# Kernel optimization log

Hardware: AMD Instinct MI355X
Metric: run time of the kernel (lower is better)

## Reference

```python
import jax, jax.numpy as jnp
import numpy as np

WIDTH = 2048
NUM_HEADS = 16
HEAD_DIM = WIDTH // NUM_HEADS  # 128
ROPE_DIMS = HEAD_DIM // 2      # 64, partial rotary
WINDOW = 512
ROPE_BASE = 10000.0
NEG_INF = -1e9


def apply_rope(x, dims, offset=0, base=ROPE_BASE):
    # x: [B, H, L, hd]; non-traditional (half-split) rotary on first `dims` dims.
    L = x.shape[2]
    half = dims // 2
    pos = (offset + jnp.arange(L)).astype(x.dtype)                     # [L]
    inv_freq = jnp.exp(-jnp.log(jnp.asarray(base, x.dtype)) * (jnp.arange(0, dims, 2).astype(x.dtype) / dims))  # [half]
    theta = pos[:, None] * inv_freq[None, :]                           # [L, half]
    cos = jnp.cos(theta)[None, None]                                   # [1,1,L,half]
    sin = jnp.sin(theta)[None, None]
    x1 = x[..., :half]
    x2 = x[..., half:dims]
    rest = x[..., dims:]
    rx1 = x1 * cos - x2 * sin
    rx2 = x1 * sin + x2 * cos
    return jnp.concatenate([rx1, rx2, rest], axis=-1)


def setup_inputs() -> dict:
    key = jax.random.key(0)
    ks = jax.random.split(key, 6)
    B, L, D, hd = 2, 2048, WIDTH, HEAD_DIM
    x = jax.random.normal(ks[0], (B, L, D), dtype=jnp.float32)
    Wq = jax.random.normal(ks[1], (D, D), dtype=jnp.float32) * 0.02
    Wk = jax.random.normal(ks[2], (D, hd), dtype=jnp.float32) * 0.02
    Wv = jax.random.normal(ks[3], (D, hd), dtype=jnp.float32) * 0.02
    Wo = jax.random.normal(ks[4], (D, D), dtype=jnp.float32) * 0.02
    bo = jax.random.normal(ks[5], (D,), dtype=jnp.float32) * 0.02
    return {"x": x, "Wq": Wq, "Wk": Wk, "Wv": Wv, "Wo": Wo, "bo": bo}


def reference(x, Wq, Wk, Wv, Wo, bo):
    B, L, D = x.shape
    H, hd = NUM_HEADS, HEAD_DIM
    scale = hd ** (-0.5)

    q = (x @ Wq).reshape(B, L, H, hd).transpose(0, 2, 1, 3)   # [B,H,L,hd]
    k = (x @ Wk).reshape(B, L, 1, hd).transpose(0, 2, 1, 3)   # [B,1,L,hd] (MQA)
    v = (x @ Wv).reshape(B, L, 1, hd).transpose(0, 2, 1, 3)

    q = apply_rope(q, ROPE_DIMS)
    k = apply_rope(k, ROPE_DIMS)

    # sliding-window causal mask: attend iff 0 <= i - j < WINDOW
    i = jnp.arange(L)[:, None]
    j = jnp.arange(L)[None, :]
    allowed = (i - j >= 0) & (i - j < WINDOW)                  # [L,L]
    mask = jnp.where(allowed, 0.0, NEG_INF).astype(x.dtype)

    scores = jnp.einsum("bhqd,bkd->bhqk", q, k[:, 0]) * scale  # [B,H,L,L]
    scores = scores + mask[None, None]
    attn = jax.nn.softmax(scores, axis=-1)
    out = jnp.einsum("bhqk,bkd->bhqd", attn, v[:, 0])          # [B,H,L,hd]
    out = out.transpose(0, 2, 1, 3).reshape(B, L, D)
    return out @ Wo + bo
```

## Files before the change

### kernel.cpp

```cpp
#include <hip/hip_runtime.h>
#include <hip/hip_bf16.h>
#include <stdint.h>


typedef float  f32x4  __attribute__((ext_vector_type(4)));
typedef __bf16 bf16x8 __attribute__((ext_vector_type(8)));

#define ASYNC_LD16(gp, lp)                                                     \
  __builtin_amdgcn_global_load_lds(                                            \
      (__attribute__((address_space(1))) void*)(gp),                           \
      (__attribute__((address_space(3))) void*)(lp), 16, 0, 0)

__global__ __launch_bounds__(256) void prep_all(
    const float* __restrict__ x, __hip_bfloat16* __restrict__ xb,
    const float* __restrict__ Wq, const float* __restrict__ Wk,
    const float* __restrict__ Wv, const float* __restrict__ Wo,
    __hip_bfloat16* __restrict__ wqkvT, __hip_bfloat16* __restrict__ woT) {
  __shared__ float t[32][33];
  int bid = blockIdx.x;
  if (bid < 8192) {
    const int i = bid * 256 + threadIdx.x;
    const float4 v = ((const float4*)x)[i];
    __align__(8) __hip_bfloat16 o[4] = {
        __float2bfloat16(v.x), __float2bfloat16(v.y),
        __float2bfloat16(v.z), __float2bfloat16(v.w)};
    *(uint2*)(xb + (size_t)i * 4) = *(uint2*)o;
    return;
  }
  bid -= 8192;
  const float* src;
  __hip_bfloat16* dst;
  int C, cb, rb;
  if (bid < 4096) {
    src = Wq; dst = wqkvT; C = 2048; cb = bid & 63; rb = bid >> 6;
  } else if (bid < 4352) {
    const int l = bid - 4096;
    src = Wk; dst = wqkvT + 2048ull * 2048; C = 128; cb = l & 3; rb = l >> 2;
  } else if (bid < 4608) {
    const int l = bid - 4352;
    src = Wv; dst = wqkvT + 2176ull * 2048; C = 128; cb = l & 3; rb = l >> 2;
  } else {
    const int l = bid - 4608;
    src = Wo; dst = woT; C = 2048; cb = l & 63; rb = l >> 6;
  }
  const int c0 = cb * 32, r0 = rb * 32;
  const int xx = threadIdx.x & 31, y = threadIdx.x >> 5;
#pragma unroll
  for (int i = 0; i < 32; i += 8)
    t[y + i][xx] = src[(size_t)(r0 + y + i) * C + c0 + xx];
  __syncthreads();
#pragma unroll
  for (int i = 0; i < 32; i += 8)
    dst[(size_t)(c0 + y + i) * 2048 + r0 + xx] = __float2bfloat16(t[xx][y + i]);
}

__device__ __forceinline__ void xcd_remap(int& bx, int& by) {
  const int nwg = gridDim.x * gridDim.y;
  const int flat = blockIdx.y * gridDim.x + blockIdx.x;
  const int cpx = nwg >> 3;
  const int nid = (flat & 7) * cpx + (flat >> 3);
  bx = nid % gridDim.x;
  by = nid / gridDim.x;
}

__device__ __forceinline__ void gemm_core64(const __bf16* __restrict__ A,
                                            const __bf16* __restrict__ BT,
                                            int K, int m0, int n0, __bf16* As,
                                            __bf16* Bs, f32x4 (&acc)[2][4]) {
  const int tid = threadIdx.x;
  const int wave = tid >> 6;
  const int lane = tid & 63;
  const int wm = (wave & 1) * 32;
  const int wn = (wave >> 1) * 64;
  const int ln = lane & 15;
  const int quad = lane >> 4;
  const int rdoff = (quad ^ ((ln >> 1) & 3)) * 8;

  size_t goffA[2];
  int ldsoffA[2];
#pragma unroll
  for (int i = 0; i < 2; i++) {
    const int cidx = (wave * 2 + i) * 64 + lane;
    const int p = cidx >> 8;
    const int pidx = cidx & 255;
    const int row = pidx >> 2;
    const int cc = pidx & 3;
    const int cg = cc ^ ((row >> 1) & 3);
    goffA[i] = (size_t)row * K + p * 32 + cg * 8;
    ldsoffA[i] = (wave * 2 + i) * 512;
  }
  size_t goffB[4];
  int ldsoffB[4];
#pragma unroll
  for (int i = 0; i < 4; i++) {
    const int cidx = (wave * 4 + i) * 64 + lane;
    const int p = cidx >> 9;
    const int pidx = cidx & 511;
    const int row = pidx >> 2;
    const int cc = pidx & 3;
    const int cg = cc ^ ((row >> 1) & 3);
    goffB[i] = (size_t)row * K + p * 32 + cg * 8;
    ldsoffB[i] = (wave * 4 + i) * 512;
  }
  const __bf16* Abase = A + (size_t)m0 * K;
  const __bf16* Bbase = BT + (size_t)n0 * K;

  for (int k0 = 0; k0 < K; k0 += 64) {
#pragma unroll
    for (int i = 0; i < 2; i++)
      ASYNC_LD16(Abase + k0 + goffA[i], As + ldsoffA[i]);
#pragma unroll
    for (int i = 0; i < 4; i++)
      ASYNC_LD16(Bbase + k0 + goffB[i], Bs + ldsoffB[i]);
    __syncthreads();
    bf16x8 af[2][2], bf[4][2];
#pragma unroll
    for (int i = 0; i < 2; i++)
#pragma unroll
      for (int p = 0; p < 2; p++)
        af[i][p] = *(const bf16x8*)&As[p * 2048 + (wm + i * 16 + ln) * 32 + rdoff];
#pragma unroll
    for (int j = 0; j < 4; j++)
#pragma unroll
      for (int p = 0; p < 2; p++)
        bf[j][p] = *(const bf16x8*)&Bs[p * 4096 + (wn + j * 16 + ln) * 32 + rdoff];
#pragma unroll
    for (int p = 0; p < 2; p++)
#pragma unroll
      for (int i = 0; i < 2; i++)
#pragma unroll
        for (int j = 0; j < 4; j++)
          acc[i][j] = __builtin_amdgcn_mfma_f32_16x16x32_bf16(af[i][p], bf[j][p],
                                                              acc[i][j], 0, 0, 0);
    __syncthreads();
  }
}

__global__ __launch_bounds__(256) void gemm_qkv(
    const __bf16* __restrict__ A, const __bf16* __restrict__ BT,
    __hip_bfloat16* __restrict__ qd, __hip_bfloat16* __restrict__ kd,
    __hip_bfloat16* __restrict__ vtd, int K) {
  __shared__ __align__(16) __bf16 As[2 * 2048];
  __shared__ __align__(16) __bf16 Bs[2 * 4096];
  int bx, by;
  xcd_remap(bx, by);
  const int m0 = by * 64;
  const int n0 = bx * 128;
  f32x4 acc[2][4];
  const f32x4 zero = {0.f, 0.f, 0.f, 0.f};
#pragma unroll
  for (int i = 0; i < 2; i++)
#pragma unroll
    for (int j = 0; j < 4; j++) acc[i][j] = zero;
  gemm_core64(A, BT, K, m0, n0, As, Bs, acc);

  const int tid = threadIdx.x;
  const int wave = tid >> 6;
  const int lane = tid & 63;
  const int quad = lane >> 4;
  const int ln = lane & 15;
  const int wm = (wave & 1) * 32;
  const int wn = (wave >> 1) * 64;

  if (n0 == 2176) {
    const int bb = m0 >> 11;
    const int mloc = m0 & 2047;
#pragma unroll
    for (int i = 0; i < 2; i++) {
      const int rb = mloc + wm + i * 16 + quad * 4;
#pragma unroll
      for (int j = 0; j < 4; j++) {
        const int col = wn + j * 16 + ln;
        __align__(8) __hip_bfloat16 t4[4];
#pragma unroll
        for (int r = 0; r < 4; r++) t4[r] = __float2bfloat16(acc[i][j][r]);
        *(uint2*)(vtd + ((size_t)(bb * 128 + col)) * 2048 + rb) = *(uint2*)t4;
      }
    }
    return;
  }

  __hip_bfloat16* dst;
  int dstride, dcol;
  if (n0 < 2048) {
    dst = qd; dstride = 2048; dcol = n0;
  } else {
    dst = kd; dstride = 128; dcol = 0;
  }
  const bool dorope = (wn == 0);
  float invf0 = 0.f, invf1 = 0.f;
  if (dorope) {
    invf0 = expf(-0.28782313662425574f * (float)ln);
    invf1 = expf(-0.28782313662425574f * (float)(16 + ln));
  }

#pragma unroll
  for (int i = 0; i < 2; i++) {
#pragma unroll
    for (int r = 0; r < 4; r++) {
      const int row = m0 + wm + i * 16 + quad * 4 + r;
      float o0 = acc[i][0][r], o1 = acc[i][1][r];
      float o2 = acc[i][2][r], o3 = acc[i][3][r];
      if (dorope) {
        const float pos = (float)(row & 2047);
        float s0, c0, s1, c1;
        __sincosf(pos * invf0, &s0, &c0);
        __sincosf(pos * invf1, &s1, &c1);
        const float a0 = o0, b0 = o2, a1 = o1, b1 = o3;
        o0 = a0 * c0 - b0 * s0;
        o2 = a0 * s0 + b0 * c0;
        o1 = a1 * c1 - b1 * s1;
        o3 = a1 * s1 + b1 * c1;
      }
      __hip_bfloat16* rp = dst + (size_t)row * dstride + dcol + wn + ln;
      rp[0]  = __float2bfloat16(o0);
      rp[16] = __float2bfloat16(o1);
      rp[32] = __float2bfloat16(o2);
      rp[48] = __float2bfloat16(o3);
    }
  }
}

__global__ __launch_bounds__(256) void gemm_out(
    const __bf16* __restrict__ A, const __bf16* __restrict__ BT,
    float* __restrict__ C, const float* __restrict__ bias, int N, int K) {
  __shared__ __align__(16) __bf16 As[2 * 2048];
  __shared__ __align__(16) __bf16 Bs[2 * 4096];
  int bx, by;
  xcd_remap(bx, by);
  const int m0 = by * 64;
  const int n0 = bx * 128;
  f32x4 acc[2][4];
  const f32x4 zero = {0.f, 0.f, 0.f, 0.f};
#pragma unroll
  for (int i = 0; i < 2; i++)
#pragma unroll
    for (int j = 0; j < 4; j++) acc[i][j] = zero;
  gemm_core64(A, BT, K, m0, n0, As, Bs, acc);

  const int tid = threadIdx.x;
  const int wave = tid >> 6;
  const int lane = tid & 63;
  const int wm = (wave & 1) * 32;
  const int wn = (wave >> 1) * 64;
  const int lrow = lane & 15;
#pragma unroll
  for (int j = 0; j < 4; j++) {
    const int col = n0 + wn + j * 16 + lrow;
    const float bv = bias[col];
#pragma unroll
    for (int i = 0; i < 2; i++) {
#pragma unroll
      for (int r = 0; r < 4; r++) {
        const int row = m0 + wm + i * 16 + (lane >> 4) * 4 + r;
        C[(size_t)row * N + col] = acc[i][j][r] + bv;
      }
    }
  }
}

__global__ __launch_bounds__(256) void attn_mfma(
    const __bf16* __restrict__ qb,
    const __bf16* __restrict__ kb,
    const __bf16* __restrict__ vtb,
    __hip_bfloat16* __restrict__ o)
{
  __shared__ __align__(16) __bf16 Ks[2][4][64 * 32];
  __shared__ __align__(16) __bf16 Vs[2][2][128 * 32];
  __shared__ __align__(16) __bf16 Ps[4][2][2][512];
  const int tid = threadIdx.x;
  const int wave = tid >> 6;
  const int lane = tid & 63;
  const int quad = lane >> 4;
  const int ln = lane & 15;
  const int bid = blockIdx.x;
  const int q0 = (bid & 15) * 128;
  const int h = (bid >> 4) & 15;
  const int b = bid >> 8;
  const int swr = (ln >> 1) & 3;
  const int rdoff = (quad ^ swr) * 8;

  bf16x8 qf[2][4];
#pragma unroll
  for (int g = 0; g < 2; g++) {
    const __bf16* qrow =
        qb + ((size_t)(b * 2048 + q0 + wave * 32 + g * 16 + ln)) * 2048 + h * 128;
#pragma unroll
    for (int ks = 0; ks < 4; ks++)
      qf[g][ks] = *(const bf16x8*)(qrow + ks * 32 + quad * 8);
  }

  f32x4 oacc[2][8];
  const f32x4 zero = {0.f, 0.f, 0.f, 0.f};
#pragma unroll
  for (int g = 0; g < 2; g++)
#pragma unroll
    for (int nb = 0; nb < 8; nb++) oacc[g][nb] = zero;
  float li[2][4] = {{0.f, 0.f, 0.f, 0.f}, {0.f, 0.f, 0.f, 0.f}};
  const float scale = 0.08838834764831845f;

  const __bf16* kbase = kb + (size_t)b * 2048 * 128;
  const __bf16* vbase = vtb + (size_t)b * 128 * 2048;

  const int key4 = lane >> 2, uu = lane & 3;
  const int sw = (key4 >> 1) & 3;

  auto stage_kv = [&](int t, int bufi) {
    const int jt = q0 - 512 + 64 * t;
#pragma unroll
    for (int i = 0; i < 4; ++i) {
      const int c = wave * 4 + i;
      const int ks = c & 3, keybase = (c >> 2) * 16;
      ASYNC_LD16(kbase + (size_t)(jt + keybase + key4) * 128 + ks * 32 +
                     (uu ^ sw) * 8,
                 &Ks[bufi][ks][keybase * 32]);
    }
#pragma unroll
    for (int i = 0; i < 4; ++i) {
      const int c = wave * 4 + i;
      const int p = c & 1, dbase = (c >> 1) * 16;
      ASYNC_LD16(vbase + (size_t)(dbase + key4) * 2048 + jt + p * 32 +
                     (uu ^ sw) * 8,
                 &Vs[bufi][p][dbase * 32]);
    }
  };

#define SOFTMAX_BODY(MASKED)                                                   \
  _Pragma("unroll") for (int g = 0; g < 2; g++)                                \
  _Pragma("unroll") for (int j = 0; j < 4; j++)                                \
  _Pragma("unroll") for (int r = 0; r < 4; r++) {                              \
    float v = sacc[g][j][r] * scale;                                           \
    if (MASKED) {                                                              \
      const int d0 = (wave * 32 + g * 16 + quad * 4 + r) - (j * 16 + ln);      \
      if (t <= 1 && d0 >= (t << 6)) v = -1e30f;                                \
      if (t >= 8 && d0 < ((t - 8) << 6)) v = -1e30f;                           \
    }                                                                          \
    v = fminf(v, 60.f);                                                        \
    const float p = __expf(v);                                                 \
    li[g][r] += p;                                                             \
    const int ch = (j & 1) * 2 + (ln >> 3);                                    \
    const int swp = (quad * 2 + (r >> 1)) & 3;                                 \
    Ps[wave][g][j >> 1][(quad * 4 + r) * 32 + (ch ^ swp) * 8 + (ln & 7)] =     \
        (__bf16)p;                                                             \
  }

  const int tstart = (q0 >= 512) ? 0 : (512 - q0) / 64;
  int cur = 0;
  stage_kv(tstart, 0);
  for (int t = tstart; t < 10; ++t) {
    __syncthreads();
    if (t + 1 < 10) stage_kv(t + 1, cur ^ 1);

    f32x4 sacc[2][4];
#pragma unroll
    for (int g = 0; g < 2; g++)
#pragma unroll
      for (int j = 0; j < 4; j++) sacc[g][j] = zero;
    __builtin_amdgcn_s_setprio(1);
#pragma unroll
    for (int j = 0; j < 4; j++)
#pragma unroll
      for (int ks = 0; ks < 4; ks++) {
        const bf16x8 kf =
            *(const bf16x8*)&Ks[cur][ks][(j * 16 + ln) * 32 + rdoff];
#pragma unroll
        for (int g = 0; g < 2; g++)
          sacc[g][j] = __builtin_amdgcn_mfma_f32_16x16x32_bf16(
              qf[g][ks], kf, sacc[g][j], 0, 0, 0);
      }
    __builtin_amdgcn_s_setprio(0);

    if (t <= 1 || t >= 8) {
      SOFTMAX_BODY(1)
    } else {
      SOFTMAX_BODY(0)
    }

    const bf16x8 pf00 = *(const bf16x8*)&Ps[wave][0][0][ln * 32 + rdoff];
    const bf16x8 pf01 = *(const bf16x8*)&Ps[wave][0][1][ln * 32 + rdoff];
    const bf16x8 pf10 = *(const bf16x8*)&Ps[wave][1][0][ln * 32 + rdoff];
    const bf16x8 pf11 = *(const bf16x8*)&Ps[wave][1][1][ln * 32 + rdoff];
    __builtin_amdgcn_s_setprio(1);
#pragma unroll
    for (int nb = 0; nb < 8; nb++) {
      const bf16x8 vf0 =
          *(const bf16x8*)&Vs[cur][0][(nb * 16 + ln) * 32 + rdoff];
      const bf16x8 vf1 =
          *(const bf16x8*)&Vs[cur][1][(nb * 16 + ln) * 32 + rdoff];
      oacc[0][nb] = __builtin_amdgcn_mfma_f32_16x16x32_bf16(pf00, vf0,
                                                            oacc[0][nb], 0, 0, 0);
      oacc[0][nb] = __builtin_amdgcn_mfma_f32_16x16x32_bf16(pf01, vf1,
                                                            oacc[0][nb], 0, 0, 0);
      oacc[1][nb] = __builtin_amdgcn_mfma_f32_16x16x32_bf16(pf10, vf0,
                                                            oacc[1][nb], 0, 0, 0);
      oacc[1][nb] = __builtin_amdgcn_mfma_f32_16x16x32_bf16(pf11, vf1,
                                                            oacc[1][nb], 0, 0, 0);
    }
    __builtin_amdgcn_s_setprio(0);
    cur ^= 1;
  }
#undef SOFTMAX_BODY

#pragma unroll
  for (int off = 1; off < 16; off <<= 1)
#pragma unroll
    for (int g = 0; g < 2; g++)
#pragma unroll
      for (int r = 0; r < 4; r++) li[g][r] += __shfl_xor(li[g][r], off);

#pragma unroll
  for (int g = 0; g < 2; g++) {
    __hip_bfloat16* obase =
        o + ((size_t)(b * 2048 + q0 + wave * 32 + g * 16 + quad * 4)) * 2048 +
        h * 128 + ln;
#pragma unroll
    for (int r = 0; r < 4; r++) {
      const float inv = 1.0f / li[g][r];
#pragma unroll
      for (int nb = 0; nb < 8; nb++)
        obase[(size_t)r * 2048 + nb * 16] = __float2bfloat16(oacc[g][nb][r] * inv);
    }
  }
}

extern "C" void kernel_launch(void* const* d_in, const int* in_sizes, int n_in,
                              void* d_out, int out_size, void* d_ws,
                              size_t ws_size, hipStream_t stream) {
  const float* x = (const float*)d_in[0];
  const float* Wq = (const float*)d_in[1];
  const float* Wk = (const float*)d_in[2];
  const float* Wv = (const float*)d_in[3];
  const float* Wo = (const float*)d_in[4];
  const float* bo = (const float*)d_in[5];
  float* out = (float*)d_out;

  char* w = (char*)d_ws;
  auto alloc = [&](size_t bytes) {
    void* p = (void*)w;
    w += (bytes + 255) & ~(size_t)255;
    return p;
  };
  __bf16* xb = (__bf16*)alloc(4096ull * 2048 * 2);
  __hip_bfloat16* wqkvT = (__hip_bfloat16*)alloc(2304ull * 2048 * 2);
  __hip_bfloat16* woT = (__hip_bfloat16*)alloc(2048ull * 2048 * 2);
  __hip_bfloat16* qbuf = (__hip_bfloat16*)alloc(4096ull * 2048 * 2);
  __hip_bfloat16* kbuf = (__hip_bfloat16*)alloc(4096ull * 128 * 2);
  __hip_bfloat16* vtb = (__hip_bfloat16*)alloc(4096ull * 128 * 2);
  __hip_bfloat16* attnb = (__hip_bfloat16*)xb;

  prep_all<<<16896, 256, 0, stream>>>(x, (__hip_bfloat16*)xb, Wq, Wk, Wv, Wo,
                                      wqkvT, woT);

  gemm_qkv<<<dim3(18, 64), 256, 0, stream>>>(xb, (const __bf16*)wqkvT, qbuf,
                                             kbuf, vtb, 2048);

  attn_mfma<<<512, 256, 0, stream>>>((const __bf16*)qbuf, (const __bf16*)kbuf,
                                     (const __bf16*)vtb, attnb);

  gemm_out<<<dim3(16, 64), 256, 0, stream>>>((const __bf16*)attnb,
                                             (const __bf16*)woT, out, bo, 2048,
                                             2048);
}
```

Before: 249.7 us.

## Switch GEMMs to 128x128 tiles with 32x32x16 MFMA and XOR-swizzled LDS

Both projection GEMMs now use 128x128 block tiles instead of 64x128. Each wave computes a 64x64 sub-tile with 32x32x16 bf16 MFMA instructions, and the LDS layout becomes a flat 64-wide row with an XOR swizzle. The epilogues (RoPE, V transpose store, bias add) are remapped to the 32x32 accumulator layout, and the grids are halved in M. The aim is more data reuse per LDS load and fewer MFMA issue slots, at the cost of fewer blocks (576 and 512) and possibly lower occupancy or wave balance on the CUs.

```diff
diff --git a/kernel.cpp b/kernel.cpp
--- a/kernel.cpp
+++ b/kernel.cpp
@@ -3,8 +3,9 @@
 #include <stdint.h>
 
 
-typedef float  f32x4  __attribute__((ext_vector_type(4)));
-typedef __bf16 bf16x8 __attribute__((ext_vector_type(8)));
+typedef float  f32x4   __attribute__((ext_vector_type(4)));
+typedef float  f32x16  __attribute__((ext_vector_type(16)));
+typedef __bf16 bf16x8  __attribute__((ext_vector_type(8)));
 
 #define ASYNC_LD16(gp, lp)                                                     \
   __builtin_amdgcn_global_load_lds(                                            \
@@ -63,75 +64,65 @@
   by = nid / gridDim.x;
 }
 
-__device__ __forceinline__ void gemm_core64(const __bf16* __restrict__ A,
+__device__ __forceinline__ void gemm_core32(const __bf16* __restrict__ A,
                                             const __bf16* __restrict__ BT,
                                             int K, int m0, int n0, __bf16* As,
-                                            __bf16* Bs, f32x4 (&acc)[2][4]) {
+                                            __bf16* Bs, f32x16 (&acc)[2][2]) {
   const int tid = threadIdx.x;
   const int wave = tid >> 6;
   const int lane = tid & 63;
-  const int wm = (wave & 1) * 32;
+  const int wm = (wave & 1) * 64;
   const int wn = (wave >> 1) * 64;
-  const int ln = lane & 15;
-  const int quad = lane >> 4;
-  const int rdoff = (quad ^ ((ln >> 1) & 3)) * 8;
-
-  size_t goffA[2];
-  int ldsoffA[2];
-#pragma unroll
-  for (int i = 0; i < 2; i++) {
-    const int cidx = (wave * 2 + i) * 64 + lane;
-    const int p = cidx >> 8;
-    const int pidx = cidx & 255;
-    const int row = pidx >> 2;
-    const int cc = pidx & 3;
-    const int cg = cc ^ ((row >> 1) & 3);
-    goffA[i] = (size_t)row * K + p * 32 + cg * 8;
-    ldsoffA[i] = (wave * 2 + i) * 512;
-  }
-  size_t goffB[4];
-  int ldsoffB[4];
+  const int l5 = lane & 31;
+  const int half = lane >> 5;
+
+  size_t goff[4];
+  int ldso[4];
 #pragma unroll
   for (int i = 0; i < 4; i++) {
-    const int cidx = (wave * 4 + i) * 64 + lane;
-    const int p = cidx >> 9;
-    const int pidx = cidx & 511;
-    const int row = pidx >> 2;
-    const int cc = pidx & 3;
-    const int cg = cc ^ ((row >> 1) & 3);
-    goffB[i] = (size_t)row * K + p * 32 + cg * 8;
-    ldsoffB[i] = (wave * 4 + i) * 512;
+    const int cidx = i * 256 + tid;
+    const int row = cidx >> 3;
+    const int c = cidx & 7;
+    const int cg = c ^ (row & 7);
+    goff[i] = (size_t)row * K + cg * 8;
+    ldso[i] = cidx * 8;
   }
   const __bf16* Abase = A + (size_t)m0 * K;
   const __bf16* Bbase = BT + (size_t)n0 * K;
 
   for (int k0 = 0; k0 < K; k0 += 64) {
 #pragma unroll
-    for (int i = 0; i < 2; i++)
-      ASYNC_LD16(Abase + k0 + goffA[i], As + ldsoffA[i]);
-#pragma unroll
     for (int i = 0; i < 4; i++)
-      ASYNC_LD16(Bbase + k0 + goffB[i], Bs + ldsoffB[i]);
+      ASYNC_LD16(Abase + k0 + goff[i], As + ldso[i]);
+#pragma unroll
+    for (int i = 0; i < 4; i++)
+      ASYNC_LD16(Bbase + k0 + goff[i], Bs + ldso[i]);
     __syncthreads();
-    bf16x8 af[2][2], bf[4][2];
-#pragma unroll
-    for (int i = 0; i < 2; i++)
-#pragma unroll
-      for (int p = 0; p < 2; p++)
-        af[i][p] = *(const bf16x8*)&As[p * 2048 + (wm + i * 16 + ln) * 32 + rdoff];
-#pragma unroll
-    for (int j = 0; j < 4; j++)
-#pragma unroll
-      for (int p = 0; p < 2; p++)
-        bf[j][p] = *(const bf16x8*)&Bs[p * 4096 + (wn + j * 16 + ln) * 32 + rdoff];
-#pragma unroll
-    for (int p = 0; p < 2; p++)
-#pragma unroll
-      for (int i = 0; i < 2; i++)
-#pragma unroll
-        for (int j = 0; j < 4; j++)
-          acc[i][j] = __builtin_amdgcn_mfma_f32_16x16x32_bf16(af[i][p], bf[j][p],
-                                                              acc[i][j], 0, 0, 0);
+    bf16x8 af[2][4], bf[2][4];
+#pragma unroll
+    for (int fi = 0; fi < 2; fi++) {
+      const int row = wm + fi * 32 + l5;
+      const int sw = row & 7;
+#pragma unroll
+      for (int s = 0; s < 4; s++)
+        af[fi][s] = *(const bf16x8*)&As[row * 64 + ((s * 2 + half) ^ sw) * 8];
+    }
+#pragma unroll
+    for (int fj = 0; fj < 2; fj++) {
+      const int row = wn + fj * 32 + l5;
+      const int sw = row & 7;
+#pragma unroll
+      for (int s = 0; s < 4; s++)
+        bf[fj][s] = *(const bf16x8*)&Bs[row * 64 + ((s * 2 + half) ^ sw) * 8];
+    }
+#pragma unroll
+    for (int s = 0; s < 4; s++)
+#pragma unroll
+      for (int fi = 0; fi < 2; fi++)
+#pragma unroll
+        for (int fj = 0; fj < 2; fj++)
+          acc[fi][fj] = __builtin_amdgcn_mfma_f32_32x32x16_bf16(
+              af[fi][s], bf[fj][s], acc[fi][fj], 0, 0, 0);
     __syncthreads();
   }
 }
@@ -140,41 +131,46 @@
     const __bf16* __restrict__ A, const __bf16* __restrict__ BT,
     __hip_bfloat16* __restrict__ qd, __hip_bfloat16* __restrict__ kd,
     __hip_bfloat16* __restrict__ vtd, int K) {
-  __shared__ __align__(16) __bf16 As[2 * 2048];
-  __shared__ __align__(16) __bf16 Bs[2 * 4096];
+  __shared__ __align__(16) __bf16 As[128 * 64];
+  __shared__ __align__(16) __bf16 Bs[128 * 64];
   int bx, by;
   xcd_remap(bx, by);
-  const int m0 = by * 64;
+  const int m0 = by * 128;
   const int n0 = bx * 128;
-  f32x4 acc[2][4];
-  const f32x4 zero = {0.f, 0.f, 0.f, 0.f};
+  f32x16 acc[2][2];
 #pragma unroll
   for (int i = 0; i < 2; i++)
 #pragma unroll
-    for (int j = 0; j < 4; j++) acc[i][j] = zero;
-  gemm_core64(A, BT, K, m0, n0, As, Bs, acc);
+    for (int j = 0; j < 2; j++)
+#pragma unroll
+      for (int e = 0; e < 16; e++) acc[i][j][e] = 0.f;
+  gemm_core32(A, BT, K, m0, n0, As, Bs, acc);
 
   const int tid = threadIdx.x;
   const int wave = tid >> 6;
   const int lane = tid & 63;
-  const int quad = lane >> 4;
-  const int ln = lane & 15;
-  const int wm = (wave & 1) * 32;
+  const int l5 = lane & 31;
+  const int half = lane >> 5;
+  const int wm = (wave & 1) * 64;
   const int wn = (wave >> 1) * 64;
 
   if (n0 == 2176) {
     const int bb = m0 >> 11;
     const int mloc = m0 & 2047;
 #pragma unroll
-    for (int i = 0; i < 2; i++) {
-      const int rb = mloc + wm + i * 16 + quad * 4;
-#pragma unroll
-      for (int j = 0; j < 4; j++) {
-        const int col = wn + j * 16 + ln;
-        __align__(8) __hip_bfloat16 t4[4];
-#pragma unroll
-        for (int r = 0; r < 4; r++) t4[r] = __float2bfloat16(acc[i][j][r]);
-        *(uint2*)(vtd + ((size_t)(bb * 128 + col)) * 2048 + rb) = *(uint2*)t4;
+    for (int fi = 0; fi < 2; fi++) {
+#pragma unroll
+      for (int fj = 0; fj < 2; fj++) {
+        const int col = wn + fj * 32 + l5;
+#pragma unroll
+        for (int vq = 0; vq < 4; vq++) {
+          const int rb = mloc + wm + fi * 32 + vq * 8 + half * 4;
+          __align__(8) __hip_bfloat16 t4[4];
+#pragma unroll
+          for (int r = 0; r < 4; r++)
+            t4[r] = __float2bfloat16(acc[fi][fj][vq * 4 + r]);
+          *(uint2*)(vtd + ((size_t)(bb * 128 + col)) * 2048 + rb) = *(uint2*)t4;
+        }
       }
     }
     return;
@@ -188,35 +184,27 @@
     dst = kd; dstride = 128; dcol = 0;
   }
   const bool dorope = (wn == 0);
-  float invf0 = 0.f, invf1 = 0.f;
-  if (dorope) {
-    invf0 = expf(-0.28782313662425574f * (float)ln);
-    invf1 = expf(-0.28782313662425574f * (float)(16 + ln));
-  }
-
-#pragma unroll
-  for (int i = 0; i < 2; i++) {
-#pragma unroll
-    for (int r = 0; r < 4; r++) {
-      const int row = m0 + wm + i * 16 + quad * 4 + r;
-      float o0 = acc[i][0][r], o1 = acc[i][1][r];
-      float o2 = acc[i][2][r], o3 = acc[i][3][r];
+  float invf = 0.f;
+  if (dorope) invf = expf(-0.28782313662425574f * (float)l5);
+
+#pragma unroll
+  for (int fi = 0; fi < 2; fi++) {
+#pragma unroll
+    for (int v = 0; v < 16; v++) {
+      const int row = m0 + wm + fi * 32 + (v & 3) + 8 * (v >> 2) + 4 * half;
+      float o0 = acc[fi][0][v];
+      float o1 = acc[fi][1][v];
       if (dorope) {
         const float pos = (float)(row & 2047);
-        float s0, c0, s1, c1;
-        __sincosf(pos * invf0, &s0, &c0);
-        __sincosf(pos * invf1, &s1, &c1);
-        const float a0 = o0, b0 = o2, a1 = o1, b1 = o3;
-        o0 = a0 * c0 - b0 * s0;
-        o2 = a0 * s0 + b0 * c0;
-        o1 = a1 * c1 - b1 * s1;
-        o3 = a1 * s1 + b1 * c1;
+        float s, c;
+        __sincosf(pos * invf, &s, &c);
+        const float a = o0, b = o1;
+        o0 = a * c - b * s;
+        o1 = a * s + b * c;
       }
-      __hip_bfloat16* rp = dst + (size_t)row * dstride + dcol + wn + ln;
+      __hip_bfloat16* rp = dst + (size_t)row * dstride + dcol + wn + l5;
       rp[0]  = __float2bfloat16(o0);
-      rp[16] = __float2bfloat16(o1);
-      rp[32] = __float2bfloat16(o2);
-      rp[48] = __float2bfloat16(o3);
+      rp[32] = __float2bfloat16(o1);
     }
   }
 }
@@ -224,36 +212,38 @@
 __global__ __launch_bounds__(256) void gemm_out(
     const __bf16* __restrict__ A, const __bf16* __restrict__ BT,
     float* __restrict__ C, const float* __restrict__ bias, int N, int K) {
-  __shared__ __align__(16) __bf16 As[2 * 2048];
-  __shared__ __align__(16) __bf16 Bs[2 * 4096];
+  __shared__ __align__(16) __bf16 As[128 * 64];
+  __shared__ __align__(16) __bf16 Bs[128 * 64];
   int bx, by;
   xcd_remap(bx, by);
-  const int m0 = by * 64;
+  const int m0 = by * 128;
   const int n0 = bx * 128;
-  f32x4 acc[2][4];
-  const f32x4 zero = {0.f, 0.f, 0.f, 0.f};
+  f32x16 acc[2][2];
 #pragma unroll
   for (int i = 0; i < 2; i++)
 #pragma unroll
-    for (int j = 0; j < 4; j++) acc[i][j] = zero;
-  gemm_core64(A, BT, K, m0, n0, As, Bs, acc);
+    for (int j = 0; j < 2; j++)
+#pragma unroll
+      for (int e = 0; e < 16; e++) acc[i][j][e] = 0.f;
+  gemm_core32(A, BT, K, m0, n0, As, Bs, acc);
 
   const int tid = threadIdx.x;
   const int wave = tid >> 6;
   const int lane = tid & 63;
-  const int wm = (wave & 1) * 32;
+  const int l5 = lane & 31;
+  const int half = lane >> 5;
+  const int wm = (wave & 1) * 64;
   const int wn = (wave >> 1) * 64;
-  const int lrow = lane & 15;
-#pragma unroll
-  for (int j = 0; j < 4; j++) {
-    const int col = n0 + wn + j * 16 + lrow;
+#pragma unroll
+  for (int fj = 0; fj < 2; fj++) {
+    const int col = n0 + wn + fj * 32 + l5;
     const float bv = bias[col];
 #pragma unroll
-    for (int i = 0; i < 2; i++) {
-#pragma unroll
-      for (int r = 0; r < 4; r++) {
-        const int row = m0 + wm + i * 16 + (lane >> 4) * 4 + r;
-        C[(size_t)row * N + col] = acc[i][j][r] + bv;
+    for (int fi = 0; fi < 2; fi++) {
+#pragma unroll
+      for (int v = 0; v < 16; v++) {
+        const int row = m0 + wm + fi * 32 + (v & 3) + 8 * (v >> 2) + 4 * half;
+        C[(size_t)row * N + col] = acc[fi][fj][v] + bv;
       }
     }
   }
@@ -451,13 +441,13 @@
   prep_all<<<16896, 256, 0, stream>>>(x, (__hip_bfloat16*)xb, Wq, Wk, Wv, Wo,
                                       wqkvT, woT);
 
-  gemm_qkv<<<dim3(18, 64), 256, 0, stream>>>(xb, (const __bf16*)wqkvT, qbuf,
+  gemm_qkv<<<dim3(18, 32), 256, 0, stream>>>(xb, (const __bf16*)wqkvT, qbuf,
                                              kbuf, vtb, 2048);
 
   attn_mfma<<<512, 256, 0, stream>>>((const __bf16*)qbuf, (const __bf16*)kbuf,
                                      (const __bf16*)vtb, attnb);
 
-  gemm_out<<<dim3(16, 64), 256, 0, stream>>>((const __bf16*)attnb,
+  gemm_out<<<dim3(16, 32), 256, 0, stream>>>((const __bf16*)attnb,
                                              (const __bf16*)woT, out, bo, 2048,
                                              2048);
 }
```

New measurement: 260.1 us. +4.1%, slower.

## Split attention block across eight waves with 16 query rows each

Applied to the files above, without the earlier changes.

The attention kernel now launches 512 threads (8 waves) per block instead of 256, and each wave handles 16 query rows instead of 32. KV staging is split so waves 0-3 load K and waves 4-7 load V, one chunk each per thread. This halves per-wave register state (accumulators, Q fragments) and adds more waves to hide latency. In exchange, each K/V LDS fragment read now feeds half as many MFMAs, and barrier cost rises with more waves per block.

```diff
diff --git a/kernel.cpp b/kernel.cpp
--- a/kernel.cpp
+++ b/kernel.cpp
@@ -259,7 +259,7 @@
   }
 }
 
-__global__ __launch_bounds__(256) void attn_mfma(
+__global__ __launch_bounds__(512) void attn_mfma(
     const __bf16* __restrict__ qb,
     const __bf16* __restrict__ kb,
     const __bf16* __restrict__ vtb,
@@ -267,9 +267,9 @@
 {
   __shared__ __align__(16) __bf16 Ks[2][4][64 * 32];
   __shared__ __align__(16) __bf16 Vs[2][2][128 * 32];
-  __shared__ __align__(16) __bf16 Ps[4][2][2][512];
+  __shared__ __align__(16) __bf16 Ps[8][2][512];
   const int tid = threadIdx.x;
-  const int wave = tid >> 6;
+  const int w = tid >> 6;
   const int lane = tid & 63;
   const int quad = lane >> 4;
   const int ln = lane & 15;
@@ -280,23 +280,20 @@
   const int swr = (ln >> 1) & 3;
   const int rdoff = (quad ^ swr) * 8;
 
-  bf16x8 qf[2][4];
-#pragma unroll
-  for (int g = 0; g < 2; g++) {
+  bf16x8 qf[4];
+  {
     const __bf16* qrow =
-        qb + ((size_t)(b * 2048 + q0 + wave * 32 + g * 16 + ln)) * 2048 + h * 128;
+        qb + ((size_t)(b * 2048 + q0 + w * 16 + ln)) * 2048 + h * 128;
 #pragma unroll
     for (int ks = 0; ks < 4; ks++)
-      qf[g][ks] = *(const bf16x8*)(qrow + ks * 32 + quad * 8);
-  }
-
-  f32x4 oacc[2][8];
+      qf[ks] = *(const bf16x8*)(qrow + ks * 32 + quad * 8);
+  }
+
+  f32x4 oacc[8];
   const f32x4 zero = {0.f, 0.f, 0.f, 0.f};
 #pragma unroll
-  for (int g = 0; g < 2; g++)
-#pragma unroll
-    for (int nb = 0; nb < 8; nb++) oacc[g][nb] = zero;
-  float li[2][4] = {{0.f, 0.f, 0.f, 0.f}, {0.f, 0.f, 0.f, 0.f}};
+  for (int nb = 0; nb < 8; nb++) oacc[nb] = zero;
+  float li[4] = {0.f, 0.f, 0.f, 0.f};
   const float scale = 0.08838834764831845f;
 
   const __bf16* kbase = kb + (size_t)b * 2048 * 128;
@@ -309,38 +306,37 @@
     const int jt = q0 - 512 + 64 * t;
 #pragma unroll
     for (int i = 0; i < 4; ++i) {
-      const int c = wave * 4 + i;
-      const int ks = c & 3, keybase = (c >> 2) * 16;
-      ASYNC_LD16(kbase + (size_t)(jt + keybase + key4) * 128 + ks * 32 +
-                     (uu ^ sw) * 8,
-                 &Ks[bufi][ks][keybase * 32]);
-    }
-#pragma unroll
-    for (int i = 0; i < 4; ++i) {
-      const int c = wave * 4 + i;
-      const int p = c & 1, dbase = (c >> 1) * 16;
-      ASYNC_LD16(vbase + (size_t)(dbase + key4) * 2048 + jt + p * 32 +
-                     (uu ^ sw) * 8,
-                 &Vs[bufi][p][dbase * 32]);
+      const int g = w * 4 + i;
+      if (g < 16) {
+        const int ks = g & 3, keybase = (g >> 2) * 16;
+        ASYNC_LD16(kbase + (size_t)(jt + keybase + key4) * 128 + ks * 32 +
+                       (uu ^ sw) * 8,
+                   &Ks[bufi][ks][keybase * 32]);
+      } else {
+        const int c = g - 16;
+        const int p = c & 1, dbase = (c >> 1) * 16;
+        ASYNC_LD16(vbase + (size_t)(dbase + key4) * 2048 + jt + p * 32 +
+                       (uu ^ sw) * 8,
+                   &Vs[bufi][p][dbase * 32]);
+      }
     }
   };
 
 #define SOFTMAX_BODY(MASKED)                                                   \
-  _Pragma("unroll") for (int g = 0; g < 2; g++)                                \
   _Pragma("unroll") for (int j = 0; j < 4; j++)                                \
   _Pragma("unroll") for (int r = 0; r < 4; r++) {                              \
-    float v = sacc[g][j][r] * scale;                                           \
+    float v = sacc[j][r] * scale;                                              \
     if (MASKED) {                                                              \
-      const int d0 = (wave * 32 + g * 16 + quad * 4 + r) - (j * 16 + ln);      \
+      const int d0 = (w * 16 + quad * 4 + r) - (j * 16 + ln);                  \
       if (t <= 1 && d0 >= (t << 6)) v = -1e30f;                                \
       if (t >= 8 && d0 < ((t - 8) << 6)) v = -1e30f;                           \
     }                                                                          \
     v = fminf(v, 60.f);                                                        \
     const float p = __expf(v);                                                 \
-    li[g][r] += p;                                                             \
+    li[r] += p;                                                                \
     const int ch = (j & 1) * 2 + (ln >> 3);                                    \
     const int swp = (quad * 2 + (r >> 1)) & 3;                                 \
-    Ps[wave][g][j >> 1][(quad * 4 + r) * 32 + (ch ^ swp) * 8 + (ln & 7)] =     \
+    Ps[w][j >> 1][(quad * 4 + r) * 32 + (ch ^ swp) * 8 + (ln & 7)] =           \
         (__bf16)p;                                                             \
   }
 
@@ -351,11 +347,9 @@
     __syncthreads();
     if (t + 1 < 10) stage_kv(t + 1, cur ^ 1);
 
-    f32x4 sacc[2][4];
-#pragma unroll
-    for (int g = 0; g < 2; g++)
-#pragma unroll
-      for (int j = 0; j < 4; j++) sacc[g][j] = zero;
+    f32x4 sacc[4];
+#pragma unroll
+    for (int j = 0; j < 4; j++) sacc[j] = zero;
     __builtin_amdgcn_s_setprio(1);
 #pragma unroll
     for (int j = 0; j < 4; j++)
@@ -363,10 +357,8 @@
       for (int ks = 0; ks < 4; ks++) {
         const bf16x8 kf =
             *(const bf16x8*)&Ks[cur][ks][(j * 16 + ln) * 32 + rdoff];
-#pragma unroll
-        for (int g = 0; g < 2; g++)
-          sacc[g][j] = __builtin_amdgcn_mfma_f32_16x16x32_bf16(
-              qf[g][ks], kf, sacc[g][j], 0, 0, 0);
+        sacc[j] = __builtin_amdgcn_mfma_f32_16x16x32_bf16(qf[ks], kf, sacc[j],
+                                                          0, 0, 0);
       }
     __builtin_amdgcn_s_setprio(0);
 
@@ -376,10 +368,8 @@
       SOFTMAX_BODY(0)
     }
 
-    const bf16x8 pf00 = *(const bf16x8*)&Ps[wave][0][0][ln * 32 + rdoff];
-    const bf16x8 pf01 = *(const bf16x8*)&Ps[wave][0][1][ln * 32 + rdoff];
-    const bf16x8 pf10 = *(const bf16x8*)&Ps[wave][1][0][ln * 32 + rdoff];
-    const bf16x8 pf11 = *(const bf16x8*)&Ps[wave][1][1][ln * 32 + rdoff];
+    const bf16x8 pf0 = *(const bf16x8*)&Ps[w][0][ln * 32 + rdoff];
+    const bf16x8 pf1 = *(const bf16x8*)&Ps[w][1][ln * 32 + rdoff];
     __builtin_amdgcn_s_setprio(1);
 #pragma unroll
     for (int nb = 0; nb < 8; nb++) {
@@ -387,14 +377,10 @@
           *(const bf16x8*)&Vs[cur][0][(nb * 16 + ln) * 32 + rdoff];
       const bf16x8 vf1 =
           *(const bf16x8*)&Vs[cur][1][(nb * 16 + ln) * 32 + rdoff];
-      oacc[0][nb] = __builtin_amdgcn_mfma_f32_16x16x32_bf16(pf00, vf0,
-                                                            oacc[0][nb], 0, 0, 0);
-      oacc[0][nb] = __builtin_amdgcn_mfma_f32_16x16x32_bf16(pf01, vf1,
-                                                            oacc[0][nb], 0, 0, 0);
-      oacc[1][nb] = __builtin_amdgcn_mfma_f32_16x16x32_bf16(pf10, vf0,
-                                                            oacc[1][nb], 0, 0, 0);
-      oacc[1][nb] = __builtin_amdgcn_mfma_f32_16x16x32_bf16(pf11, vf1,
-                                                            oacc[1][nb], 0, 0, 0);
+      oacc[nb] = __builtin_amdgcn_mfma_f32_16x16x32_bf16(pf0, vf0, oacc[nb],
+                                                         0, 0, 0);
+      oacc[nb] = __builtin_amdgcn_mfma_f32_16x16x32_bf16(pf1, vf1, oacc[nb],
+                                                         0, 0, 0);
     }
     __builtin_amdgcn_s_setprio(0);
     cur ^= 1;
@@ -404,22 +390,16 @@
 #pragma unroll
   for (int off = 1; off < 16; off <<= 1)
 #pragma unroll
-    for (int g = 0; g < 2; g++)
-#pragma unroll
-      for (int r = 0; r < 4; r++) li[g][r] += __shfl_xor(li[g][r], off);
-
-#pragma unroll
-  for (int g = 0; g < 2; g++) {
-    __hip_bfloat16* obase =
-        o + ((size_t)(b * 2048 + q0 + wave * 32 + g * 16 + quad * 4)) * 2048 +
-        h * 128 + ln;
-#pragma unroll
-    for (int r = 0; r < 4; r++) {
-      const float inv = 1.0f / li[g][r];
-#pragma unroll
-      for (int nb = 0; nb < 8; nb++)
-        obase[(size_t)r * 2048 + nb * 16] = __float2bfloat16(oacc[g][nb][r] * inv);
-    }
+    for (int r = 0; r < 4; r++) li[r] += __shfl_xor(li[r], off);
+
+  __hip_bfloat16* obase =
+      o + ((size_t)(b * 2048 + q0 + w * 16 + quad * 4)) * 2048 + h * 128 + ln;
+#pragma unroll
+  for (int r = 0; r < 4; r++) {
+    const float inv = 1.0f / li[r];
+#pragma unroll
+    for (int nb = 0; nb < 8; nb++)
+      obase[(size_t)r * 2048 + nb * 16] = __float2bfloat16(oacc[nb][r] * inv);
   }
 }
 
@@ -454,7 +434,7 @@
   gemm_qkv<<<dim3(18, 64), 256, 0, stream>>>(xb, (const __bf16*)wqkvT, qbuf,
                                              kbuf, vtb, 2048);
 
-  attn_mfma<<<512, 256, 0, stream>>>((const __bf16*)qbuf, (const __bf16*)kbuf,
+  attn_mfma<<<512, 512, 0, stream>>>((const __bf16*)qbuf, (const __bf16*)kbuf,
                                      (const __bf16*)vtb, attnb);
 
   gemm_out<<<dim3(16, 64), 256, 0, stream>>>((const __bf16*)attnb,
```

After: 248.7 us. Within noise of the previous version (-0.4%).
